# Kernel tuning notes

Measured on AMD Instinct MI355X. Metric: run time of the kernel, lower is better.

## Reference

```python
import jax, jax.numpy as jnp
import numpy as np

M, B, E, A = 3, 65536, 512, 256  # modalities, batch, embedding_dim, attention_dim
LN_EPS = 1e-5


def setup_inputs() -> dict:
    key = jax.random.key(0)
    ks = jax.random.split(key, 9)
    s_e = 1.0 / np.sqrt(E)
    s_a = 1.0 / np.sqrt(A)
    return {
        "x": jax.random.normal(ks[0], (M, B, E), jnp.float32),
        "Wq": jax.random.normal(ks[1], (M, E, A), jnp.float32) * s_e,
        "bq": jax.random.normal(ks[2], (M, A), jnp.float32) * s_e,
        "Wk": jax.random.normal(ks[3], (M, E, A), jnp.float32) * s_e,
        "bk": jax.random.normal(ks[4], (M, A), jnp.float32) * s_e,
        "v": jax.random.normal(ks[5], (M, A), jnp.float32) * s_a,
        "Wt": jax.random.normal(ks[6], (M, M, E, E), jnp.float32) * s_e,
        "bt": jax.random.normal(ks[7], (M, M, E), jnp.float32) * s_e,
        "gamma": jnp.ones((M * E,), jnp.float32),
        "beta": jnp.zeros((M * E,), jnp.float32),
    }


def reference(x, Wq, bq, Wk, bk, v, Wt, bt, gamma, beta):
    # Per-modality query/key projections (batched over modality axis m).
    qp = jnp.einsum('mbe,mea->mba', x, Wq) + bq[:, None, :]  # [M,B,A]
    kp = jnp.einsum('mbe,mea->mba', x, Wk) + bk[:, None, :]  # [M,B,A]
    # Additive score: v_q^T tanh(q_proj[q] + k_proj[k]) for every (q,k) pair.
    t = jnp.tanh(qp[:, None, :, :] + kp[None, :, :, :])       # [Q,K,B,A]
    scores = jnp.einsum('qa,qkba->qkb', v, t)                  # [Q,K,B]
    # Exclude k == q from the softmax (torch code skips key_mod == query_mod).
    diag = jnp.eye(scores.shape[0], dtype=bool)[:, :, None]
    scores = jnp.where(diag, -jnp.inf, scores)
    alpha = jax.nn.softmax(scores, axis=1)                     # [Q,K,B], zero on diag
    # Weighted sum of per-pair linear transforms of the key embeddings.
    att = (jnp.einsum('qkb,kbe,qkef->qbf', alpha, x, Wt)
           + jnp.einsum('qkb,qke->qbe', alpha, bt))            # [Q,B,E]
    attended = x + att                                         # residual per modality
    # Concat modalities along features, then LayerNorm over M*E.
    fused = jnp.transpose(attended, (1, 0, 2)).reshape(x.shape[1], -1)  # [B, M*E]
    mu = jnp.mean(fused, axis=-1, keepdims=True)
    var = jnp.var(fused, axis=-1, keepdims=True)
    fused = (fused - mu) * jax.lax.rsqrt(var + LN_EPS) * gamma + beta
    return fused
```

## Files before the change

### kernel.cpp

```cpp
#include <hip/hip_runtime.h>
#include <hip/hip_bf16.h>

#define MOD   3
#define BATCH 65536
#define EDIM  512
#define ADIM  256
#define FEAT  1536

typedef __attribute__((ext_vector_type(8))) short   s16x8;
typedef __attribute__((ext_vector_type(8))) __bf16  bf16x8;
typedef __attribute__((ext_vector_type(4))) float   f32x4;
typedef __attribute__((ext_vector_type(4))) unsigned short u16x4;

__device__ __forceinline__ float b2f(unsigned short u) {
    union { unsigned int ui; float f; } c; c.ui = ((unsigned int)u) << 16; return c.f;
}
__device__ __forceinline__ unsigned short f2b(float f) {
    __hip_bfloat16 h = __float2bfloat16(f);
    return __builtin_bit_cast(unsigned short, h);
}

__device__ __forceinline__ void glds16(const unsigned short* g, unsigned short* l) {
    __builtin_amdgcn_global_load_lds(
        (const __attribute__((address_space(1))) void*)g,
        (__attribute__((address_space(3))) void*)l, 16, 0, 0);
}

#define WAITV(N) asm volatile("s_waitcnt vmcnt(%0)" :: "i"(N) : "memory")
__device__ __forceinline__ void BAR() {
    asm volatile("" ::: "memory");
    __builtin_amdgcn_s_barrier();
    asm volatile("" ::: "memory");
}

__global__ __launch_bounds__(256) void k_convert_x(const float* __restrict__ x,
                                                   unsigned short* __restrict__ xb, int n4) {
    int i = blockIdx.x * blockDim.x + threadIdx.x;
    int stride = gridDim.x * blockDim.x;
    for (; i < n4; i += stride) {
        f32x4 v = *((const f32x4*)x + i);
        u16x4 o;
        for (int j = 0; j < 4; ++j) o[j] = f2b(v[j]);
        *((u16x4*)xb + i) = o;
    }
}

__global__ __launch_bounds__(256) void k_prep_w(const float* __restrict__ Wq,
                                                const float* __restrict__ Wk,
                                                const float* __restrict__ Wt,
                                                unsigned short* __restrict__ wqk,
                                                unsigned short* __restrict__ wtt3) {
    int i = blockIdx.x * blockDim.x + threadIdx.x;
    int stride = gridDim.x * blockDim.x;
    for (int idx = i; idx < MOD * EDIM * EDIM; idx += stride) {
        int m = idx / (EDIM * EDIM); int r = idx % (EDIM * EDIM);
        int n = r / EDIM; int e = r % EDIM;
        float f = (n < ADIM) ? Wq[(m * EDIM + e) * ADIM + n]
                             : Wk[(m * EDIM + e) * ADIM + (n - ADIM)];
        wqk[idx] = f2b(f);
    }
    for (int idx = i; idx < MOD * 1024 * EDIM; idx += stride) {
        int q = idx / (1024 * EDIM); int r = idx % (1024 * EDIM);
        int n = r / EDIM; int e = r % EDIM;
        int kp = n >> 9, f = n & 511;
        int k = (q + 1 + kp) % 3;
        wtt3[idx] = f2b(Wt[((size_t)(q * 3 + k) * EDIM + e) * EDIM + f]);
    }
}


struct GCtx {
    const unsigned short* pA[2];
    const unsigned short* pB[2];
    const unsigned short* lds;
    unsigned short* ldsW;
    int aoff, boff;
};

__device__ __forceinline__ void gctx_init(GCtx& c,
                                          const unsigned short* Ag0, const unsigned short* Ag1,
                                          const unsigned short* Bg0, const unsigned short* Bg1,
                                          unsigned short* lds) {
    const int tid = threadIdx.x, lane = tid & 63, wid = tid >> 6;
    const int wm = wid >> 2, wn = wid & 3;
    int stageRow = wid * 32 + (lane >> 2);
    int gsrc8 = ((lane & 3) ^ ((lane >> 3) & 3)) * 8;
    size_t so = (size_t)stageRow * 512 + gsrc8;
    c.pA[0] = Ag0 + so; c.pA[1] = Ag1 + so;
    c.pB[0] = Bg0 + so; c.pB[1] = Bg1 + so;
    c.lds = lds;
    c.ldsW = lds + wid * 1024;
    int swz8 = ((lane >> 4) ^ ((lane >> 1) & 3)) * 8;
    c.aoff = (wm * 128 + (lane & 15)) * 32 + swz8;
    c.boff = (wn * 64 + (lane & 15)) * 32 + swz8;
}

template<int NU>
__device__ __forceinline__ void stage_s(const GCtx& c, int s) {
    if (s >= NU) return;
    int p = s >> 5;
    int sp = s & 31;
    int colK = (sp >> 2) * 64 + (sp & 2) * 16;
    const unsigned short* src = ((sp & 1) ? c.pB[p] : c.pA[p]) + colK;
    unsigned short* dst = c.ldsW + (s & 7) * 8192;
    glds16(src, dst);
    glds16(src + 16 * 512, dst + 512);
}

template<int W, int NU>
__device__ __forceinline__ void window2(int T, int ks, const GCtx& c, f32x4 (&acc)[8][4]) {
    int u0 = 4 * T + 2 * ks;
    const unsigned short* Asl = c.lds + (size_t)(u0 & 7) * 8192;
    const unsigned short* Bsl = c.lds + (size_t)((u0 + 1) & 7) * 8192;
    s16x8 af[8], bf[4];
#pragma unroll
    for (int j = 0; j < 4; ++j) bf[j] = *(const s16x8*)(Bsl + c.boff + j * 512);
#pragma unroll
    for (int i = 0; i < 8; ++i) af[i] = *(const s16x8*)(Asl + c.aoff + i * 512);
    stage_s<NU>(c, u0 + 4);
    stage_s<NU>(c, u0 + 5);
    WAITV(W);
    BAR();
    __builtin_amdgcn_s_setprio(1);
#pragma unroll
    for (int i = 0; i < 8; ++i)
#pragma unroll
        for (int j = 0; j < 4; ++j)
            acc[i][j] = __builtin_amdgcn_mfma_f32_16x16x32_bf16(
                __builtin_bit_cast(bf16x8, af[i]), __builtin_bit_cast(bf16x8, bf[j]),
                acc[i][j], 0, 0, 0);
    __builtin_amdgcn_s_setprio(0);
    BAR();
}

template<int NU>
__device__ __forceinline__ void pipe_prologue2(const GCtx& c) {
#pragma unroll
    for (int s = 0; s < 4; ++s) stage_s<NU>(c, s);
    WAITV(4);
    BAR();
}

__global__ __launch_bounds__(512, 2) void k_gemm_proj(const unsigned short* __restrict__ xb,
                                                      const unsigned short* __restrict__ wqk,
                                                      const float* __restrict__ bq,
                                                      const float* __restrict__ bk,
                                                      unsigned short* __restrict__ proj) {
    __shared__ __align__(16) unsigned short LDS[65536];
    int l = (blockIdx.x & 7) * 192 + (blockIdx.x >> 3);
    int ct = l & 1, rt = (l >> 1) & 255, m = l >> 9;
    int row0 = rt * 256, col0 = ct * 256;
    f32x4 acc[8][4];
#pragma unroll
    for (int i = 0; i < 8; ++i) for (int j = 0; j < 4; ++j) acc[i][j] = (f32x4)0.f;
    GCtx c;
    const unsigned short* Ag = xb + ((size_t)m * BATCH + row0) * EDIM;
    const unsigned short* Bg = wqk + ((size_t)m * EDIM + col0) * EDIM;
    gctx_init(c, Ag, Ag, Bg, Bg, LDS);
    pipe_prologue2<32>(c);
#pragma unroll 1
    for (int t = 0; t < 7; ++t) {
        window2<4, 32>(t, 0, c, acc);
        window2<4, 32>(t, 1, c, acc);
    }
    window2<0, 32>(7, 0, c, acc);
    window2<0, 32>(7, 1, c, acc);
    int lane = threadIdx.x & 63, wid = threadIdx.x >> 6;
    int wm = wid >> 2, wn = wid & 3;
#pragma unroll
    for (int j = 0; j < 4; ++j) {
        int col = col0 + wn * 64 + j * 16 + (lane & 15);
        float bias = (col < ADIM) ? bq[m * ADIM + col] : bk[m * ADIM + col - ADIM];
#pragma unroll
        for (int i8 = 0; i8 < 8; ++i8) {
            int rbase = row0 + wm * 128 + i8 * 16 + (lane >> 4) * 4;
#pragma unroll
            for (int r = 0; r < 4; ++r)
                proj[((size_t)m * BATCH + rbase + r) * EDIM + col] = f2b(acc[i8][j][r] + bias);
        }
    }
}

__global__ __launch_bounds__(256) void k_scores(const unsigned short* __restrict__ proj,
                                                const float* __restrict__ v,
                                                float* __restrict__ alpha) {
    int wid = threadIdx.x >> 6, lane = threadIdx.x & 63;
    size_t b = (size_t)blockIdx.x * 4 + wid;
    float qp[3][4], kp[3][4], vq[3][4];
    for (int m = 0; m < 3; ++m) {
        const unsigned short* p = proj + ((size_t)m * BATCH + b) * EDIM;
        u16x4 uq = *(const u16x4*)(p + lane * 4);
        u16x4 uk = *(const u16x4*)(p + ADIM + lane * 4);
        f32x4 vv = *((const f32x4*)(v + m * ADIM) + lane);
        for (int j = 0; j < 4; ++j) { qp[m][j] = b2f(uq[j]); kp[m][j] = b2f(uk[j]); vq[m][j] = vv[j]; }
    }
    for (int q = 0; q < 3; ++q) {
        float s[2];
        for (int ki = 0; ki < 2; ++ki) {
            int k = (q + 1 + ki) % 3;
            float a = 0.f;
            for (int j = 0; j < 4; ++j) a += vq[q][j] * tanhf(qp[q][j] + kp[k][j]);
            for (int off = 32; off; off >>= 1) a += __shfl_xor(a, off, 64);
            s[ki] = a;
        }
        if (lane == 0) {
            float mx = fmaxf(s[0], s[1]);
            float e0 = expf(s[0] - mx), e1 = expf(s[1] - mx);
            float inv = 1.f / (e0 + e1);
            alpha[(size_t)(q * 2 + 0) * BATCH + b] = e0 * inv;
            alpha[(size_t)(q * 2 + 1) * BATCH + b] = e1 * inv;
        }
    }
}

__global__ __launch_bounds__(512, 2) void k_gemm_att(const unsigned short* __restrict__ xb,
                                                     const unsigned short* __restrict__ wtt3,
                                                     const float* __restrict__ alpha,
                                                     const float* __restrict__ bt,
                                                     unsigned short* __restrict__ att) {
    __shared__ __align__(16) unsigned short LDS[65536];
    __shared__ float auxA0[256], auxA1[256], auxR[256];
    int l = (blockIdx.x & 7) * 192 + (blockIdx.x >> 3);
    int ct = l & 1, rt = (l >> 1) & 255, q = l >> 9;
    int row0 = rt * 256, col0 = ct * 256;
    int kA = (q + 1) % 3, kB = (q + 2) % 3;
    int tid = threadIdx.x, lane = tid & 63, wid = tid >> 6;
    int wm = wid >> 2, wn = wid & 3;

    if (tid < 256) {
        float a0 = alpha[(size_t)(q * 2 + 0) * BATCH + row0 + tid];
        float a1 = alpha[(size_t)(q * 2 + 1) * BATCH + row0 + tid];
        auxA0[tid] = a0; auxA1[tid] = a1;
        auxR[tid] = a0 / fmaxf(a1, 1e-30f);
    }
    __syncthreads();

    f32x4 acc[8][4];
#pragma unroll
    for (int i = 0; i < 8; ++i) for (int j = 0; j < 4; ++j) acc[i][j] = (f32x4)0.f;
    GCtx c;
    gctx_init(c,
              xb + ((size_t)kA * BATCH + row0) * EDIM,
              xb + ((size_t)kB * BATCH + row0) * EDIM,
              wtt3 + ((size_t)(q * 2 + 0) * EDIM + col0) * EDIM,
              wtt3 + ((size_t)(q * 2 + 1) * EDIM + col0) * EDIM,
              LDS);
    pipe_prologue2<64>(c);
#pragma unroll 1
    for (int t = 0; t < 8; ++t) {
        window2<4, 64>(t, 0, c, acc);
        window2<4, 64>(t, 1, c, acc);
    }
#pragma unroll
    for (int i8 = 0; i8 < 8; ++i8) {
        int rl = wm * 128 + i8 * 16 + (lane >> 4) * 4;
        f32x4 rv = *(const f32x4*)&auxR[rl];
#pragma unroll
        for (int j = 0; j < 4; ++j)
#pragma unroll
            for (int r = 0; r < 4; ++r) acc[i8][j][r] *= rv[r];
    }
#pragma unroll 1
    for (int t = 8; t < 15; ++t) {
        window2<4, 64>(t, 0, c, acc);
        window2<4, 64>(t, 1, c, acc);
    }
    window2<0, 64>(15, 0, c, acc);
    window2<0, 64>(15, 1, c, acc);

    float btAv[4], btBv[4];
#pragma unroll
    for (int j = 0; j < 4; ++j) {
        int col = col0 + wn * 64 + j * 16 + (lane & 15);
        btAv[j] = bt[(size_t)(q * 3 + kA) * EDIM + col];
        btBv[j] = bt[(size_t)(q * 3 + kB) * EDIM + col];
    }
#pragma unroll
    for (int i8 = 0; i8 < 8; ++i8) {
        int rl = wm * 128 + i8 * 16 + (lane >> 4) * 4;
        f32x4 a0v = *(const f32x4*)&auxA0[rl];
        f32x4 a1v = *(const f32x4*)&auxA1[rl];
        int rbase = row0 + rl;
#pragma unroll
        for (int j = 0; j < 4; ++j) {
            int col = col0 + wn * 64 + j * 16 + (lane & 15);
#pragma unroll
            for (int r = 0; r < 4; ++r)
                att[((size_t)q * BATCH + rbase + r) * EDIM + col] =
                    f2b(a1v[r] * acc[i8][j][r] + a0v[r] * btAv[j] + a1v[r] * btBv[j]);
        }
    }
}

__global__ __launch_bounds__(192) void k_fuse_ln(const unsigned short* __restrict__ xb,
                                                 const unsigned short* __restrict__ att,
                                                 const float* __restrict__ gamma,
                                                 const float* __restrict__ beta,
                                                 float* __restrict__ out) {
    __shared__ float red[2][3];
    int b = blockIdx.x, t = threadIdx.x, m = t >> 6, lane = t & 63;
    int e0 = lane * 8;
    s16x8 xv = *(const s16x8*)(xb + ((size_t)m * BATCH + b) * EDIM + e0);
    s16x8 av = *(const s16x8*)(att + ((size_t)m * BATCH + b) * EDIM + e0);
    float v[8]; float s = 0.f, s2 = 0.f;
#pragma unroll
    for (int j = 0; j < 8; ++j) {
        float vv = b2f((unsigned short)xv[j]) + b2f((unsigned short)av[j]);
        v[j] = vv; s += vv; s2 += vv * vv;
    }
    for (int off = 32; off; off >>= 1) { s += __shfl_xor(s, off, 64); s2 += __shfl_xor(s2, off, 64); }
    if (lane == 0) { red[0][m] = s; red[1][m] = s2; }
    __syncthreads();
    float S = red[0][0] + red[0][1] + red[0][2];
    float S2 = red[1][0] + red[1][1] + red[1][2];
    float mu  = S * (1.f / 1536.f);
    float var = S2 * (1.f / 1536.f) - mu * mu;
    float rs  = rsqrtf(var + 1e-5f);
    int f0 = m * EDIM + e0;
    f32x4 g0 = *(const f32x4*)(gamma + f0), g1 = *(const f32x4*)(gamma + f0 + 4);
    f32x4 be0 = *(const f32x4*)(beta + f0), be1 = *(const f32x4*)(beta + f0 + 4);
    f32x4 o0, o1;
#pragma unroll
    for (int j = 0; j < 4; ++j) {
        o0[j] = (v[j]     - mu) * rs * g0[j] + be0[j];
        o1[j] = (v[j + 4] - mu) * rs * g1[j] + be1[j];
    }
    float* op = out + (size_t)b * FEAT + f0;
    *(f32x4*)op = o0; *(f32x4*)(op + 4) = o1;
}

extern "C" void kernel_launch(void* const* d_in, const int* in_sizes, int n_in,
                              void* d_out, int out_size, void* d_ws, size_t ws_size,
                              hipStream_t stream) {
    const float* x     = (const float*)d_in[0];
    const float* Wq    = (const float*)d_in[1];
    const float* bq    = (const float*)d_in[2];
    const float* Wk    = (const float*)d_in[3];
    const float* bk    = (const float*)d_in[4];
    const float* v     = (const float*)d_in[5];
    const float* Wt    = (const float*)d_in[6];
    const float* bt    = (const float*)d_in[7];
    const float* gamma = (const float*)d_in[8];
    const float* beta  = (const float*)d_in[9];
    float* out = (float*)d_out;

    char* ws = (char*)d_ws;
    unsigned short* wqk   = (unsigned short*)(ws);
    unsigned short* wtt3  = (unsigned short*)(ws + 1572864);
    float*          alpha = (float*)        (ws + 4718592);
    unsigned short* xb    = (unsigned short*)(ws + 6291456);
    unsigned short* att   = (unsigned short*)(ws + 207618048);
    unsigned short* proj  = att;

    k_convert_x<<<4096, 256, 0, stream>>>(x, xb, (MOD * BATCH * EDIM) / 4);
    k_prep_w   <<<2048, 256, 0, stream>>>(Wq, Wk, Wt, wqk, wtt3);
    k_gemm_proj<<<1536, 512, 0, stream>>>(xb, wqk, bq, bk, proj);
    k_scores   <<<16384, 256, 0, stream>>>(proj, v, alpha);
    k_gemm_att <<<1536, 512, 0, stream>>>(xb, wtt3, alpha, bt, att);
    k_fuse_ln  <<<65536, 192, 0, stream>>>(xb, att, gamma, beta, out);
}
```

Measured before the change: 777.0 us.

## Double-buffer LDS fragments in GEMM pipelines and make LayerNorm one wave per row

The GEMM main loops now register-double-buffer the A/B fragments. Each window issues LDS reads for the next window before running the MFMAs of the current one, and global-to-LDS staging runs one step further ahead (prologue of six stages). The intent is to hide LDS read latency behind matrix math and keep fewer barriers per window. Separately, the fused LayerNorm kernel now assigns one wavefront per batch row covering all three modalities, which removes shared-memory reduction and the block barrier and packs eight rows per block. This costs more registers for the doubled fragment arrays and depends on the LDS ring indexing staying correct.

```diff
diff --git a/kernel.cpp b/kernel.cpp
--- a/kernel.cpp
+++ b/kernel.cpp
@@ -107,38 +107,59 @@
     glds16(src + 16 * 512, dst + 512);
 }
 
-template<int W, int NU>
-__device__ __forceinline__ void window2(int T, int ks, const GCtx& c, f32x4 (&acc)[8][4]) {
-    int u0 = 4 * T + 2 * ks;
-    const unsigned short* Asl = c.lds + (size_t)(u0 & 7) * 8192;
-    const unsigned short* Bsl = c.lds + (size_t)((u0 + 1) & 7) * 8192;
-    s16x8 af[8], bf[4];
-#pragma unroll
-    for (int j = 0; j < 4; ++j) bf[j] = *(const s16x8*)(Bsl + c.boff + j * 512);
-#pragma unroll
-    for (int i = 0; i < 8; ++i) af[i] = *(const s16x8*)(Asl + c.aoff + i * 512);
-    stage_s<NU>(c, u0 + 4);
-    stage_s<NU>(c, u0 + 5);
-    WAITV(W);
+template<int W4, int WAIT, bool DOREAD, int NU>
+__device__ __forceinline__ void window_i(int w, const GCtx& c,
+                                         s16x8 (&afC)[8], s16x8 (&bfC)[4],
+                                         s16x8 (&afN)[8], s16x8 (&bfN)[4],
+                                         f32x4 (&acc)[8][4]) {
+    WAITV(WAIT);
     BAR();
-    __builtin_amdgcn_s_setprio(1);
+    if constexpr (DOREAD) {
+        const unsigned short* Asl = c.lds + (size_t)((2 * W4 + 2) & 7) * 8192;
+        const unsigned short* Bsl = c.lds + (size_t)((2 * W4 + 3) & 7) * 8192;
+#pragma unroll
+        for (int j = 0; j < 4; ++j) bfN[j] = *(const s16x8*)(Bsl + c.boff + j * 512);
+#pragma unroll
+        for (int i = 0; i < 8; ++i) afN[i] = *(const s16x8*)(Asl + c.aoff + i * 512);
+    }
+    stage_s<NU>(c, 2 * w + 6);
+    stage_s<NU>(c, 2 * w + 7);
 #pragma unroll
     for (int i = 0; i < 8; ++i)
 #pragma unroll
         for (int j = 0; j < 4; ++j)
             acc[i][j] = __builtin_amdgcn_mfma_f32_16x16x32_bf16(
-                __builtin_bit_cast(bf16x8, af[i]), __builtin_bit_cast(bf16x8, bf[j]),
+                __builtin_bit_cast(bf16x8, afC[i]), __builtin_bit_cast(bf16x8, bfC[j]),
                 acc[i][j], 0, 0, 0);
-    __builtin_amdgcn_s_setprio(0);
+}
+
+template<bool LAST, int NU>
+__device__ __forceinline__ void do_quad(int w0, const GCtx& c,
+                                        s16x8 (&af0)[8], s16x8 (&bf0)[4],
+                                        s16x8 (&af1)[8], s16x8 (&bf1)[4],
+                                        f32x4 (&acc)[8][4]) {
+    window_i<0, 4, true, NU>(w0 + 0, c, af0, bf0, af1, bf1, acc);
+    window_i<1, 4, true, NU>(w0 + 1, c, af1, bf1, af0, bf0, acc);
+    window_i<2, LAST ? 0 : 4, true, NU>(w0 + 2, c, af0, bf0, af1, bf1, acc);
+    if constexpr (LAST)
+        window_i<3, 0, false, NU>(w0 + 3, c, af1, bf1, af0, bf0, acc);
+    else
+        window_i<3, 4, true, NU>(w0 + 3, c, af1, bf1, af0, bf0, acc);
+}
+
+template<int NU>
+__device__ __forceinline__ void pipe_prologue3(const GCtx& c,
+                                               s16x8 (&af0)[8], s16x8 (&bf0)[4]) {
+#pragma unroll
+    for (int s = 0; s < 6; ++s) stage_s<NU>(c, s);
+    WAITV(8);
     BAR();
-}
-
-template<int NU>
-__device__ __forceinline__ void pipe_prologue2(const GCtx& c) {
-#pragma unroll
-    for (int s = 0; s < 4; ++s) stage_s<NU>(c, s);
-    WAITV(4);
-    BAR();
+    const unsigned short* Asl = c.lds;
+    const unsigned short* Bsl = c.lds + 8192;
+#pragma unroll
+    for (int j = 0; j < 4; ++j) bf0[j] = *(const s16x8*)(Bsl + c.boff + j * 512);
+#pragma unroll
+    for (int i = 0; i < 8; ++i) af0[i] = *(const s16x8*)(Asl + c.aoff + i * 512);
 }
 
 __global__ __launch_bounds__(512, 2) void k_gemm_proj(const unsigned short* __restrict__ xb,
@@ -157,14 +178,12 @@
     const unsigned short* Ag = xb + ((size_t)m * BATCH + row0) * EDIM;
     const unsigned short* Bg = wqk + ((size_t)m * EDIM + col0) * EDIM;
     gctx_init(c, Ag, Ag, Bg, Bg, LDS);
-    pipe_prologue2<32>(c);
+    s16x8 af0[8], af1[8], bf0[4], bf1[4];
+    pipe_prologue3<32>(c, af0, bf0);
 #pragma unroll 1
-    for (int t = 0; t < 7; ++t) {
-        window2<4, 32>(t, 0, c, acc);
-        window2<4, 32>(t, 1, c, acc);
-    }
-    window2<0, 32>(7, 0, c, acc);
-    window2<0, 32>(7, 1, c, acc);
+    for (int qd = 0; qd < 3; ++qd)
+        do_quad<false, 32>(4 * qd, c, af0, bf0, af1, bf1, acc);
+    do_quad<true, 32>(12, c, af0, bf0, af1, bf1, acc);
     int lane = threadIdx.x & 63, wid = threadIdx.x >> 6;
     int wm = wid >> 2, wn = wid & 3;
 #pragma unroll
@@ -245,12 +264,11 @@
               wtt3 + ((size_t)(q * 2 + 0) * EDIM + col0) * EDIM,
               wtt3 + ((size_t)(q * 2 + 1) * EDIM + col0) * EDIM,
               LDS);
-    pipe_prologue2<64>(c);
+    s16x8 af0[8], af1[8], bf0[4], bf1[4];
+    pipe_prologue3<64>(c, af0, bf0);
 #pragma unroll 1
-    for (int t = 0; t < 8; ++t) {
-        window2<4, 64>(t, 0, c, acc);
-        window2<4, 64>(t, 1, c, acc);
-    }
+    for (int qd = 0; qd < 4; ++qd)
+        do_quad<false, 64>(4 * qd, c, af0, bf0, af1, bf1, acc);
 #pragma unroll
     for (int i8 = 0; i8 < 8; ++i8) {
         int rl = wm * 128 + i8 * 16 + (lane >> 4) * 4;
@@ -261,12 +279,9 @@
             for (int r = 0; r < 4; ++r) acc[i8][j][r] *= rv[r];
     }
 #pragma unroll 1
-    for (int t = 8; t < 15; ++t) {
-        window2<4, 64>(t, 0, c, acc);
-        window2<4, 64>(t, 1, c, acc);
-    }
-    window2<0, 64>(15, 0, c, acc);
-    window2<0, 64>(15, 1, c, acc);
+    for (int qd = 4; qd < 7; ++qd)
+        do_quad<false, 64>(4 * qd, c, af0, bf0, af1, bf1, acc);
+    do_quad<true, 64>(28, c, af0, bf0, af1, bf1, acc);
 
     float btAv[4], btBv[4];
 #pragma unroll
@@ -292,41 +307,45 @@
     }
 }
 
-__global__ __launch_bounds__(192) void k_fuse_ln(const unsigned short* __restrict__ xb,
+__global__ __launch_bounds__(512) void k_fuse_ln(const unsigned short* __restrict__ xb,
                                                  const unsigned short* __restrict__ att,
                                                  const float* __restrict__ gamma,
                                                  const float* __restrict__ beta,
                                                  float* __restrict__ out) {
-    __shared__ float red[2][3];
-    int b = blockIdx.x, t = threadIdx.x, m = t >> 6, lane = t & 63;
+    int lane = threadIdx.x & 63, w = threadIdx.x >> 6;
+    size_t b = (size_t)blockIdx.x * 8 + w;
     int e0 = lane * 8;
-    s16x8 xv = *(const s16x8*)(xb + ((size_t)m * BATCH + b) * EDIM + e0);
-    s16x8 av = *(const s16x8*)(att + ((size_t)m * BATCH + b) * EDIM + e0);
-    float v[8]; float s = 0.f, s2 = 0.f;
-#pragma unroll
-    for (int j = 0; j < 8; ++j) {
-        float vv = b2f((unsigned short)xv[j]) + b2f((unsigned short)av[j]);
-        v[j] = vv; s += vv; s2 += vv * vv;
+    float v[3][8];
+    float s = 0.f, s2 = 0.f;
+#pragma unroll
+    for (int m = 0; m < 3; ++m) {
+        size_t off = ((size_t)m * BATCH + b) * EDIM + e0;
+        s16x8 xv = *(const s16x8*)(xb + off);
+        s16x8 av = *(const s16x8*)(att + off);
+#pragma unroll
+        for (int j = 0; j < 8; ++j) {
+            float vv = b2f((unsigned short)xv[j]) + b2f((unsigned short)av[j]);
+            v[m][j] = vv; s += vv; s2 += vv * vv;
+        }
     }
     for (int off = 32; off; off >>= 1) { s += __shfl_xor(s, off, 64); s2 += __shfl_xor(s2, off, 64); }
-    if (lane == 0) { red[0][m] = s; red[1][m] = s2; }
-    __syncthreads();
-    float S = red[0][0] + red[0][1] + red[0][2];
-    float S2 = red[1][0] + red[1][1] + red[1][2];
-    float mu  = S * (1.f / 1536.f);
-    float var = S2 * (1.f / 1536.f) - mu * mu;
+    float mu  = s * (1.f / 1536.f);
+    float var = s2 * (1.f / 1536.f) - mu * mu;
     float rs  = rsqrtf(var + 1e-5f);
-    int f0 = m * EDIM + e0;
-    f32x4 g0 = *(const f32x4*)(gamma + f0), g1 = *(const f32x4*)(gamma + f0 + 4);
-    f32x4 be0 = *(const f32x4*)(beta + f0), be1 = *(const f32x4*)(beta + f0 + 4);
-    f32x4 o0, o1;
-#pragma unroll
-    for (int j = 0; j < 4; ++j) {
-        o0[j] = (v[j]     - mu) * rs * g0[j] + be0[j];
-        o1[j] = (v[j + 4] - mu) * rs * g1[j] + be1[j];
-    }
-    float* op = out + (size_t)b * FEAT + f0;
-    *(f32x4*)op = o0; *(f32x4*)(op + 4) = o1;
+#pragma unroll
+    for (int m = 0; m < 3; ++m) {
+        int f0 = m * EDIM + e0;
+        f32x4 g0 = *(const f32x4*)(gamma + f0), g1 = *(const f32x4*)(gamma + f0 + 4);
+        f32x4 be0 = *(const f32x4*)(beta + f0), be1 = *(const f32x4*)(beta + f0 + 4);
+        f32x4 o0, o1;
+#pragma unroll
+        for (int j = 0; j < 4; ++j) {
+            o0[j] = (v[m][j]     - mu) * rs * g0[j] + be0[j];
+            o1[j] = (v[m][j + 4] - mu) * rs * g1[j] + be1[j];
+        }
+        float* op = out + (size_t)b * FEAT + f0;
+        *(f32x4*)op = o0; *(f32x4*)(op + 4) = o1;
+    }
 }
 
 extern "C" void kernel_launch(void* const* d_in, const int* in_sizes, int n_in,
@@ -357,5 +376,5 @@
     k_gemm_proj<<<1536, 512, 0, stream>>>(xb, wqk, bq, bk, proj);
     k_scores   <<<16384, 256, 0, stream>>>(proj, v, alpha);
     k_gemm_att <<<1536, 512, 0, stream>>>(xb, wtt3, alpha, bt, att);
-    k_fuse_ln  <<<65536, 192, 0, stream>>>(xb, att, gamma, beta, out);
-}
+    k_fuse_ln  <<<8192, 512, 0, stream>>>(xb, att, gamma, beta, out);
+}
```

Measured after the change: 858.7 us. 1.11x slower.

## Replace pipelined 256x256 GEMM with simple 128x128 single-buffered tiles

Applied to the files above, without the earlier changes.

Both GEMM kernels (projection and attention transform) switch from 256x256 block tiles with an 8-stage LDS ring prefetch to 128x128 tiles with 4 warps and a single LDS buffer per operand, synchronised twice per K step. Grids grow fourfold and launch bounds target three blocks per CU. The intent is presumably higher occupancy and simpler scheduling. In exchange, load/compute overlap is lost and per-tile reuse drops, so global traffic rises.

```diff
diff --git a/kernel.cpp b/kernel.cpp
--- a/kernel.cpp
+++ b/kernel.cpp
@@ -24,13 +24,6 @@
     __builtin_amdgcn_global_load_lds(
         (const __attribute__((address_space(1))) void*)g,
         (__attribute__((address_space(3))) void*)l, 16, 0, 0);
-}
-
-#define WAITV(N) asm volatile("s_waitcnt vmcnt(%0)" :: "i"(N) : "memory")
-__device__ __forceinline__ void BAR() {
-    asm volatile("" ::: "memory");
-    __builtin_amdgcn_s_barrier();
-    asm volatile("" ::: "memory");
 }
 
 __global__ __launch_bounds__(256) void k_convert_x(const float* __restrict__ x,
@@ -69,114 +62,87 @@
 }
 
 
-struct GCtx {
-    const unsigned short* pA[2];
-    const unsigned short* pB[2];
-    const unsigned short* lds;
-    unsigned short* ldsW;
+struct G1 {
+    const unsigned short* sA[2];
+    const unsigned short* sB[2];
+    unsigned short *As, *Bs;
+    unsigned short *dA, *dB;
     int aoff, boff;
 };
 
-__device__ __forceinline__ void gctx_init(GCtx& c,
-                                          const unsigned short* Ag0, const unsigned short* Ag1,
-                                          const unsigned short* Bg0, const unsigned short* Bg1,
-                                          unsigned short* lds) {
+__device__ __forceinline__ void g1_init(G1& g,
+                                        const unsigned short* Ag0, const unsigned short* Ag1,
+                                        const unsigned short* Bg0, const unsigned short* Bg1,
+                                        unsigned short* As, unsigned short* Bs) {
     const int tid = threadIdx.x, lane = tid & 63, wid = tid >> 6;
-    const int wm = wid >> 2, wn = wid & 3;
-    int stageRow = wid * 32 + (lane >> 2);
-    int gsrc8 = ((lane & 3) ^ ((lane >> 3) & 3)) * 8;
-    size_t so = (size_t)stageRow * 512 + gsrc8;
-    c.pA[0] = Ag0 + so; c.pA[1] = Ag1 + so;
-    c.pB[0] = Bg0 + so; c.pB[1] = Bg1 + so;
-    c.lds = lds;
-    c.ldsW = lds + wid * 1024;
-    int swz8 = ((lane >> 4) ^ ((lane >> 1) & 3)) * 8;
-    c.aoff = (wm * 128 + (lane & 15)) * 32 + swz8;
-    c.boff = (wn * 64 + (lane & 15)) * 32 + swz8;
-}
-
-template<int NU>
-__device__ __forceinline__ void stage_s(const GCtx& c, int s) {
-    if (s >= NU) return;
-    int p = s >> 5;
-    int sp = s & 31;
-    int colK = (sp >> 2) * 64 + (sp & 2) * 16;
-    const unsigned short* src = ((sp & 1) ? c.pB[p] : c.pA[p]) + colK;
-    unsigned short* dst = c.ldsW + (s & 7) * 8192;
-    glds16(src, dst);
-    glds16(src + 16 * 512, dst + 512);
-}
-
-template<int W, int NU>
-__device__ __forceinline__ void window2(int T, int ks, const GCtx& c, f32x4 (&acc)[8][4]) {
-    int u0 = 4 * T + 2 * ks;
-    const unsigned short* Asl = c.lds + (size_t)(u0 & 7) * 8192;
-    const unsigned short* Bsl = c.lds + (size_t)((u0 + 1) & 7) * 8192;
-    s16x8 af[8], bf[4];
-#pragma unroll
-    for (int j = 0; j < 4; ++j) bf[j] = *(const s16x8*)(Bsl + c.boff + j * 512);
-#pragma unroll
-    for (int i = 0; i < 8; ++i) af[i] = *(const s16x8*)(Asl + c.aoff + i * 512);
-    stage_s<NU>(c, u0 + 4);
-    stage_s<NU>(c, u0 + 5);
-    WAITV(W);
-    BAR();
-    __builtin_amdgcn_s_setprio(1);
-#pragma unroll
-    for (int i = 0; i < 8; ++i)
+    const int wm = wid >> 1, wn = wid & 1;
+    int srow = wid * 32 + (lane >> 2);
+    int g8 = ((lane & 3) ^ ((lane >> 3) & 3)) * 8;
+    size_t so = (size_t)srow * 512 + g8;
+    g.sA[0] = Ag0 + so; g.sA[1] = Ag1 + so;
+    g.sB[0] = Bg0 + so; g.sB[1] = Bg1 + so;
+    g.As = As; g.Bs = Bs;
+    g.dA = As + wid * 1024;
+    g.dB = Bs + wid * 1024;
+    int rr = lane & 15, cg = lane >> 4;
+    int swz8 = (cg ^ ((lane >> 1) & 3)) * 8;
+    g.aoff = (wm * 64 + rr) * 32 + swz8;
+    g.boff = (wn * 64 + rr) * 32 + swz8;
+}
+
+template<int P>
+__device__ __forceinline__ void g1_step(const G1& g, int kt, f32x4 (&acc)[4][4]) {
+    const unsigned short* a = g.sA[P] + kt * 32;
+    const unsigned short* b = g.sB[P] + kt * 32;
+    glds16(a, g.dA); glds16(a + 16 * 512, g.dA + 512);
+    glds16(b, g.dB); glds16(b + 16 * 512, g.dB + 512);
+    __syncthreads();
+    s16x8 af[4], bf[4];
+#pragma unroll
+    for (int i = 0; i < 4; ++i) af[i] = *(const s16x8*)(g.As + g.aoff + i * 512);
+#pragma unroll
+    for (int j = 0; j < 4; ++j) bf[j] = *(const s16x8*)(g.Bs + g.boff + j * 512);
+#pragma unroll
+    for (int i = 0; i < 4; ++i)
 #pragma unroll
         for (int j = 0; j < 4; ++j)
             acc[i][j] = __builtin_amdgcn_mfma_f32_16x16x32_bf16(
                 __builtin_bit_cast(bf16x8, af[i]), __builtin_bit_cast(bf16x8, bf[j]),
                 acc[i][j], 0, 0, 0);
-    __builtin_amdgcn_s_setprio(0);
-    BAR();
-}
-
-template<int NU>
-__device__ __forceinline__ void pipe_prologue2(const GCtx& c) {
-#pragma unroll
-    for (int s = 0; s < 4; ++s) stage_s<NU>(c, s);
-    WAITV(4);
-    BAR();
-}
-
-__global__ __launch_bounds__(512, 2) void k_gemm_proj(const unsigned short* __restrict__ xb,
+    __syncthreads();
+}
+
+__global__ __launch_bounds__(256, 3) void k_gemm_proj(const unsigned short* __restrict__ xb,
                                                       const unsigned short* __restrict__ wqk,
                                                       const float* __restrict__ bq,
                                                       const float* __restrict__ bk,
                                                       unsigned short* __restrict__ proj) {
-    __shared__ __align__(16) unsigned short LDS[65536];
-    int l = (blockIdx.x & 7) * 192 + (blockIdx.x >> 3);
-    int ct = l & 1, rt = (l >> 1) & 255, m = l >> 9;
-    int row0 = rt * 256, col0 = ct * 256;
-    f32x4 acc[8][4];
-#pragma unroll
-    for (int i = 0; i < 8; ++i) for (int j = 0; j < 4; ++j) acc[i][j] = (f32x4)0.f;
-    GCtx c;
+    __shared__ __align__(16) unsigned short As[4096];
+    __shared__ __align__(16) unsigned short Bs[4096];
+    int l = (blockIdx.x & 7) * 768 + (blockIdx.x >> 3);
+    int ct = l & 3, rt = (l >> 2) & 511, m = l >> 11;
+    int row0 = rt * 128, col0 = ct * 128;
+    f32x4 acc[4][4];
+#pragma unroll
+    for (int i = 0; i < 4; ++i) for (int j = 0; j < 4; ++j) acc[i][j] = (f32x4)0.f;
+    G1 g;
     const unsigned short* Ag = xb + ((size_t)m * BATCH + row0) * EDIM;
     const unsigned short* Bg = wqk + ((size_t)m * EDIM + col0) * EDIM;
-    gctx_init(c, Ag, Ag, Bg, Bg, LDS);
-    pipe_prologue2<32>(c);
+    g1_init(g, Ag, Ag, Bg, Bg, As, Bs);
 #pragma unroll 1
-    for (int t = 0; t < 7; ++t) {
-        window2<4, 32>(t, 0, c, acc);
-        window2<4, 32>(t, 1, c, acc);
-    }
-    window2<0, 32>(7, 0, c, acc);
-    window2<0, 32>(7, 1, c, acc);
+    for (int kt = 0; kt < 16; ++kt) g1_step<0>(g, kt, acc);
     int lane = threadIdx.x & 63, wid = threadIdx.x >> 6;
-    int wm = wid >> 2, wn = wid & 3;
+    int wm = wid >> 1, wn = wid & 1;
 #pragma unroll
     for (int j = 0; j < 4; ++j) {
         int col = col0 + wn * 64 + j * 16 + (lane & 15);
         float bias = (col < ADIM) ? bq[m * ADIM + col] : bk[m * ADIM + col - ADIM];
 #pragma unroll
-        for (int i8 = 0; i8 < 8; ++i8) {
-            int rbase = row0 + wm * 128 + i8 * 16 + (lane >> 4) * 4;
+        for (int i = 0; i < 4; ++i) {
+            int rbase = row0 + wm * 64 + i * 16 + (lane >> 4) * 4;
 #pragma unroll
             for (int r = 0; r < 4; ++r)
-                proj[((size_t)m * BATCH + rbase + r) * EDIM + col] = f2b(acc[i8][j][r] + bias);
+                proj[((size_t)m * BATCH + rbase + r) * EDIM + col] = f2b(acc[i][j][r] + bias);
         }
     }
 }
@@ -213,21 +179,22 @@
     }
 }
 
-__global__ __launch_bounds__(512, 2) void k_gemm_att(const unsigned short* __restrict__ xb,
+__global__ __launch_bounds__(256, 3) void k_gemm_att(const unsigned short* __restrict__ xb,
                                                      const unsigned short* __restrict__ wtt3,
                                                      const float* __restrict__ alpha,
                                                      const float* __restrict__ bt,
                                                      unsigned short* __restrict__ att) {
-    __shared__ __align__(16) unsigned short LDS[65536];
-    __shared__ float auxA0[256], auxA1[256], auxR[256];
-    int l = (blockIdx.x & 7) * 192 + (blockIdx.x >> 3);
-    int ct = l & 1, rt = (l >> 1) & 255, q = l >> 9;
-    int row0 = rt * 256, col0 = ct * 256;
+    __shared__ __align__(16) unsigned short As[4096];
+    __shared__ __align__(16) unsigned short Bs[4096];
+    __shared__ float auxA0[128], auxA1[128], auxR[128];
+    int l = (blockIdx.x & 7) * 768 + (blockIdx.x >> 3);
+    int ct = l & 3, rt = (l >> 2) & 511, q = l >> 11;
+    int row0 = rt * 128, col0 = ct * 128;
     int kA = (q + 1) % 3, kB = (q + 2) % 3;
     int tid = threadIdx.x, lane = tid & 63, wid = tid >> 6;
-    int wm = wid >> 2, wn = wid & 3;
-
-    if (tid < 256) {
+    int wm = wid >> 1, wn = wid & 1;
+
+    if (tid < 128) {
         float a0 = alpha[(size_t)(q * 2 + 0) * BATCH + row0 + tid];
         float a1 = alpha[(size_t)(q * 2 + 1) * BATCH + row0 + tid];
         auxA0[tid] = a0; auxA1[tid] = a1;
@@ -235,38 +202,29 @@
     }
     __syncthreads();
 
-    f32x4 acc[8][4];
-#pragma unroll
-    for (int i = 0; i < 8; ++i) for (int j = 0; j < 4; ++j) acc[i][j] = (f32x4)0.f;
-    GCtx c;
-    gctx_init(c,
-              xb + ((size_t)kA * BATCH + row0) * EDIM,
-              xb + ((size_t)kB * BATCH + row0) * EDIM,
-              wtt3 + ((size_t)(q * 2 + 0) * EDIM + col0) * EDIM,
-              wtt3 + ((size_t)(q * 2 + 1) * EDIM + col0) * EDIM,
-              LDS);
-    pipe_prologue2<64>(c);
+    f32x4 acc[4][4];
+#pragma unroll
+    for (int i = 0; i < 4; ++i) for (int j = 0; j < 4; ++j) acc[i][j] = (f32x4)0.f;
+    G1 g;
+    g1_init(g,
+            xb + ((size_t)kA * BATCH + row0) * EDIM,
+            xb + ((size_t)kB * BATCH + row0) * EDIM,
+            wtt3 + ((size_t)(q * 2 + 0) * EDIM + col0) * EDIM,
+            wtt3 + ((size_t)(q * 2 + 1) * EDIM + col0) * EDIM,
+            As, Bs);
 #pragma unroll 1
-    for (int t = 0; t < 8; ++t) {
-        window2<4, 64>(t, 0, c, acc);
-        window2<4, 64>(t, 1, c, acc);
-    }
-#pragma unroll
-    for (int i8 = 0; i8 < 8; ++i8) {
-        int rl = wm * 128 + i8 * 16 + (lane >> 4) * 4;
+    for (int kt = 0; kt < 16; ++kt) g1_step<0>(g, kt, acc);
+#pragma unroll
+    for (int i = 0; i < 4; ++i) {
+        int rl = wm * 64 + i * 16 + (lane >> 4) * 4;
         f32x4 rv = *(const f32x4*)&auxR[rl];
 #pragma unroll
         for (int j = 0; j < 4; ++j)
 #pragma unroll
-            for (int r = 0; r < 4; ++r) acc[i8][j][r] *= rv[r];
+            for (int r = 0; r < 4; ++r) acc[i][j][r] *= rv[r];
     }
 #pragma unroll 1
-    for (int t = 8; t < 15; ++t) {
-        window2<4, 64>(t, 0, c, acc);
-        window2<4, 64>(t, 1, c, acc);
-    }
-    window2<0, 64>(15, 0, c, acc);
-    window2<0, 64>(15, 1, c, acc);
+    for (int kt = 0; kt < 16; ++kt) g1_step<1>(g, kt, acc);
 
     float btAv[4], btBv[4];
 #pragma unroll
@@ -276,8 +234,8 @@
         btBv[j] = bt[(size_t)(q * 3 + kB) * EDIM + col];
     }
 #pragma unroll
-    for (int i8 = 0; i8 < 8; ++i8) {
-        int rl = wm * 128 + i8 * 16 + (lane >> 4) * 4;
+    for (int i = 0; i < 4; ++i) {
+        int rl = wm * 64 + i * 16 + (lane >> 4) * 4;
         f32x4 a0v = *(const f32x4*)&auxA0[rl];
         f32x4 a1v = *(const f32x4*)&auxA1[rl];
         int rbase = row0 + rl;
@@ -287,7 +245,7 @@
 #pragma unroll
             for (int r = 0; r < 4; ++r)
                 att[((size_t)q * BATCH + rbase + r) * EDIM + col] =
-                    f2b(a1v[r] * acc[i8][j][r] + a0v[r] * btAv[j] + a1v[r] * btBv[j]);
+                    f2b(a1v[r] * acc[i][j][r] + a0v[r] * btAv[j] + a1v[r] * btBv[j]);
         }
     }
 }
@@ -354,8 +312,8 @@
 
     k_convert_x<<<4096, 256, 0, stream>>>(x, xb, (MOD * BATCH * EDIM) / 4);
     k_prep_w   <<<2048, 256, 0, stream>>>(Wq, Wk, Wt, wqk, wtt3);
-    k_gemm_proj<<<1536, 512, 0, stream>>>(xb, wqk, bq, bk, proj);
+    k_gemm_proj<<<6144, 256, 0, stream>>>(xb, wqk, bq, bk, proj);
     k_scores   <<<16384, 256, 0, stream>>>(proj, v, alpha);
-    k_gemm_att <<<1536, 512, 0, stream>>>(xb, wtt3, alpha, bt, att);
+    k_gemm_att <<<6144, 256, 0, stream>>>(xb, wtt3, alpha, bt, att);
     k_fuse_ln  <<<65536, 192, 0, stream>>>(xb, att, gamma, beta, out);
 }
```

Result: no change. 766.7 us (-1.3%).
